# Kernel optimization log

Measured on AMD Instinct MI355X. Metric: run time of the kernel, lower is better.

Reference implementation:

```python
import jax, jax.numpy as jnp
import numpy as np

N_NODES = 100000
MAX_DEG = 128
BATCH = 16384
NUM_SAMPLES = 25


def setup_inputs() -> dict:
    key = jax.random.key(0)
    k1, k2, k3 = jax.random.split(key, 3)
    adj_weight = jax.random.uniform(k1, (N_NODES, MAX_DEG), dtype=jnp.float32)
    adj_info = jax.random.randint(k2, (N_NODES, MAX_DEG), 0, N_NODES, dtype=jnp.int32)
    ids = jax.random.randint(k3, (BATCH,), 0, N_NODES, dtype=jnp.int64)
    return {
        "adj_weight": adj_weight,
        "adj_info": adj_info,
        "ids": ids,
        "num_samples": NUM_SAMPLES,
    }


def reference(adj_weight, adj_info, ids, num_samples):
    # Gather per-node neighbor lists and weights: [B, max_deg]
    adj_lists = adj_info[ids]
    adj_weight_lists = adj_weight[ids]
    # tf.multinomial(tf.log(w), num_samples): categorical sampling with
    # replacement, probabilities proportional to weights.
    logits = jnp.log(adj_weight_lists)  # [B, max_deg]
    skey = jax.random.key(42)
    # categorical over last axis; draw num_samples per row -> [B, num_samples]
    idx = jax.random.categorical(
        skey, logits, axis=-1, shape=(num_samples, ids.shape[0])
    ).T
    # Gather sampled neighbor ids (equivalent to the flattened bias+gather trick)
    res = jnp.take_along_axis(adj_lists, idx, axis=1)  # [B, num_samples]
    return res
```

## Files before the change

kernel.cpp:

```cpp
#include <hip/hip_runtime.h>
#include <stdint.h>


#define MAXDEG 128

__device__ __forceinline__ uint32_t rotl32(uint32_t x, int r) {
  return __builtin_rotateleft32(x, r);
}

__device__ __forceinline__ uint32_t tf_bits(uint32_t i) {
  uint32_t x0, x1;
  x1 = i + 42u;
  x0 = x1;
  x1 = rotl32(x1, 13) ^ x0;
  x0 += x1; x1 = rotl32(x1, 15) ^ x0;
  x0 += x1; x1 = rotl32(x1, 26) ^ x0;
  x0 += x1; x1 = rotl32(x1,  6) ^ x0;
  x1 += 0x1BD11BF1u; x0 = x0 + x1 + 42u;
  x1 = rotl32(x1, 17) ^ x0;
  x0 += x1; x1 = rotl32(x1, 29) ^ x0;
  x0 += x1; x1 = rotl32(x1, 16) ^ x0;
  x0 += x1; x1 = rotl32(x1, 24) ^ x0;
  x1 += 2u; x0 = x0 + x1 + 0x1BD11BF0u;
  x1 = rotl32(x1, 13) ^ x0;
  x0 += x1; x1 = rotl32(x1, 15) ^ x0;
  x0 += x1; x1 = rotl32(x1, 26) ^ x0;
  x0 += x1; x1 = rotl32(x1,  6) ^ x0;
  x1 += 45u; x0 = x0 + x1;
  x1 = rotl32(x1, 17) ^ x0;
  x0 += x1; x1 = rotl32(x1, 29) ^ x0;
  x0 += x1; x1 = rotl32(x1, 16) ^ x0;
  x0 += x1; x1 = rotl32(x1, 24) ^ x0;
  x1 += 0x1BD11BF4u; x0 = x0 + x1 + 42u;
  x1 = rotl32(x1, 13) ^ x0;
  x0 += x1; x1 = rotl32(x1, 15) ^ x0;
  x0 += x1; x1 = rotl32(x1, 26) ^ x0;
  x0 += x1; x1 = rotl32(x1,  6) ^ x0;
  return (x0 + 0x1BD11BF0u) ^ (x1 + 5u);
}

__device__ __forceinline__ float uniform_from_bits(uint32_t bits) {
  uint32_t fb = (bits >> 9) | 0x3f800000u;
  float f = __uint_as_float(fb) - 1.0f;
  return fmaxf(f, 1.17549435e-38f);
}

__device__ __forceinline__ float zscore(float lwp, uint32_t bits) {
  const float l = __log2f(uniform_from_bits(bits));
  const float t = __log2f(-l);
  return __builtin_fmaf(-0.69314718056f, t, lwp);
}

#define SWZMAX(zm, pat) \
  zm = fmaxf(zm, __int_as_float(__builtin_amdgcn_ds_swizzle(__float_as_int(zm), (pat))))

__global__ __launch_bounds__(256) void wns_kernel(
    const float* __restrict__ adj_weight,
    const int* __restrict__ adj_info,
    const int* __restrict__ ids,
    int* __restrict__ out,
    int batch, int nsamp) {
  const int lane = threadIdx.x & 63;
  const int l = lane & 31;
  const int wid = blockIdx.x * 4 + (threadIdx.x >> 6);
  if (2 * wid >= batch) return;
  const int b = 2 * wid + (lane >> 5);

  const long long nid = (long long)ids[b];
  const float4 wv = *(const float4*)(adj_weight + nid * MAXDEG + 4 * l);
  const float lwp0 = __logf(wv.x) + 0.36651292f;
  const float lwp1 = __logf(wv.y) + 0.36651292f;
  const float lwp2 = __logf(wv.z) + 0.36651292f;
  const float lwp3 = __logf(wv.w) + 0.36651292f;

  uint32_t sbase = (uint32_t)b * 128u + (uint32_t)(4 * l);
  const uint32_t sstep = (uint32_t)batch * 128u;

  #pragma unroll 2
  for (int s = 0; s < nsamp; ++s, sbase += sstep) {
    const uint32_t bits0 = tf_bits(sbase + 0u);
    const uint32_t bits1 = tf_bits(sbase + 1u);
    const uint32_t bits2 = tf_bits(sbase + 2u);
    const uint32_t bits3 = tf_bits(sbase + 3u);

    const float z0 = zscore(lwp0, bits0);
    const float z1 = zscore(lwp1, bits1);
    const float z2 = zscore(lwp2, bits2);
    const float z3 = zscore(lwp3, bits3);

    float zmax = fmaxf(fmaxf(fmaxf(z0, z1), z2), z3);
    SWZMAX(zmax, 0x041F);
    SWZMAX(zmax, 0x081F);
    SWZMAX(zmax, 0x101F);
    SWZMAX(zmax, 0x201F);
    SWZMAX(zmax, 0x401F);

    const float thr = zmax - 3.0e-4f;
    const unsigned long long m0 = __ballot(z0 > thr);
    const unsigned long long m1 = __ballot(z1 > thr);
    const unsigned long long m2 = __ballot(z2 > thr);
    const unsigned long long m3 = __ballot(z3 > thr);
    const uint32_t a0 = (uint32_t)m0, a1 = (uint32_t)m1,
                   a2 = (uint32_t)m2, a3 = (uint32_t)m3;
    const uint32_t c0 = (uint32_t)(m0 >> 32), c1 = (uint32_t)(m1 >> 32),
                   c2 = (uint32_t)(m2 >> 32), c3 = (uint32_t)(m3 >> 32);
    const int cntA = __popc(a0) + __popc(a1) + __popc(a2) + __popc(a3);
    const int cntB = __popc(c0) + __popc(c1) + __popc(c2) + __popc(c3);

    int d;
    if (cntA == 1 && cntB == 1) {
      const int dA = a0 ? 4 * __builtin_ctz(a0)
                   : a1 ? 4 * __builtin_ctz(a1) + 1
                   : a2 ? 4 * __builtin_ctz(a2) + 2
                        : 4 * __builtin_ctz(a3) + 3;
      const int dB = c0 ? 4 * __builtin_ctz(c0)
                   : c1 ? 4 * __builtin_ctz(c1) + 1
                   : c2 ? 4 * __builtin_ctz(c2) + 2
                        : 4 * __builtin_ctz(c3) + 3;
      d = (lane < 32) ? dA : dB;
    } else {
      double bz = log((double)wv.x) - log(-log((double)uniform_from_bits(bits0)));
      int bd = 4 * l;
      const double Z1 = log((double)wv.y) - log(-log((double)uniform_from_bits(bits1)));
      if (Z1 > bz) { bz = Z1; bd = 4 * l + 1; }
      const double Z2 = log((double)wv.z) - log(-log((double)uniform_from_bits(bits2)));
      if (Z2 > bz) { bz = Z2; bd = 4 * l + 2; }
      const double Z3 = log((double)wv.w) - log(-log((double)uniform_from_bits(bits3)));
      if (Z3 > bz) { bz = Z3; bd = 4 * l + 3; }
      #pragma unroll
      for (int m = 1; m < 32; m <<= 1) {
        const double oz = __shfl_xor(bz, m);
        const int od = __shfl_xor(bd, m);
        if (oz > bz || (oz == bz && od < bd)) { bz = oz; bd = od; }
      }
      d = bd;
    }

    if (l == 0) {
      out[(long long)b * nsamp + s] = adj_info[nid * MAXDEG + d];
    }
  }
}

extern "C" void kernel_launch(void* const* d_in, const int* in_sizes, int n_in,
                              void* d_out, int out_size, void* d_ws, size_t ws_size,
                              hipStream_t stream) {
  const float* adj_weight = (const float*)d_in[0];
  const int* adj_info = (const int*)d_in[1];
  const int* ids = (const int*)d_in[2];
  int batch = in_sizes[2];
  int nsamp = out_size / batch;
  int waves = (batch + 1) / 2;
  int blocks = (waves + 3) / 4;
  wns_kernel<<<blocks, 256, 0, stream>>>(adj_weight, adj_info, ids,
                                         (int*)d_out, batch, nsamp);
}
```

Before: 153.4 us.

## Defer fp64 tie-break to noinline post-loop pass and use DPP reductions

```diff
diff --git a/kernel.cpp b/kernel.cpp
--- a/kernel.cpp
+++ b/kernel.cpp
@@ -51,10 +51,43 @@
   return __builtin_fmaf(-0.69314718056f, t, lwp);
 }
 
-#define SWZMAX(zm, pat) \
-  zm = fmaxf(zm, __int_as_float(__builtin_amdgcn_ds_swizzle(__float_as_int(zm), (pat))))
+template <int CTRL>
+__device__ __forceinline__ float dpp_max_step(float z) {
+  const int t = __builtin_amdgcn_update_dpp(0, __float_as_int(z), CTRL, 0xF, 0xF, true);
+  return fmaxf(z, __int_as_float(t));
+}
 
-__global__ __launch_bounds__(256) void wns_kernel(
+__device__ __forceinline__ float swz_max16(float z) {
+  return fmaxf(z, __int_as_float(
+      __builtin_amdgcn_ds_swizzle(__float_as_int(z), 0x401F)));
+}
+
+__device__ __attribute__((noinline)) void resolve_f64(
+    float4 wv, uint32_t sbase, int l, int lane, int storeLane,
+    const int* __restrict__ adj_info, long long nid,
+    int* __restrict__ out, long long outIdx) {
+  const uint32_t bits0 = tf_bits(sbase + 0u);
+  const uint32_t bits1 = tf_bits(sbase + 1u);
+  const uint32_t bits2 = tf_bits(sbase + 2u);
+  const uint32_t bits3 = tf_bits(sbase + 3u);
+  double bz = log((double)wv.x) - log(-log((double)uniform_from_bits(bits0)));
+  int bd = 4 * l;
+  const double Z1 = log((double)wv.y) - log(-log((double)uniform_from_bits(bits1)));
+  if (Z1 > bz) { bz = Z1; bd = 4 * l + 1; }
+  const double Z2 = log((double)wv.z) - log(-log((double)uniform_from_bits(bits2)));
+  if (Z2 > bz) { bz = Z2; bd = 4 * l + 2; }
+  const double Z3 = log((double)wv.w) - log(-log((double)uniform_from_bits(bits3)));
+  if (Z3 > bz) { bz = Z3; bd = 4 * l + 3; }
+  #pragma unroll
+  for (int m = 1; m < 32; m <<= 1) {
+    const double oz = __shfl_xor(bz, m);
+    const int od = __shfl_xor(bd, m);
+    if (oz > bz || (oz == bz && od < bd)) { bz = oz; bd = od; }
+  }
+  if (lane == storeLane) out[outIdx] = adj_info[nid * MAXDEG + bd];
+}
+
+__global__ __launch_bounds__(256, 8) void wns_kernel(
     const float* __restrict__ adj_weight,
     const int* __restrict__ adj_info,
     const int* __restrict__ ids,
@@ -76,7 +109,9 @@
   uint32_t sbase = (uint32_t)b * 128u + (uint32_t)(4 * l);
   const uint32_t sstep = (uint32_t)batch * 128u;
 
-  #pragma unroll 2
+  uint32_t flagA = 0u, flagB = 0u;
+
+  #pragma unroll 5
   for (int s = 0; s < nsamp; ++s, sbase += sstep) {
     const uint32_t bits0 = tf_bits(sbase + 0u);
     const uint32_t bits1 = tf_bits(sbase + 1u);
@@ -89,11 +124,11 @@
     const float z3 = zscore(lwp3, bits3);
 
     float zmax = fmaxf(fmaxf(fmaxf(z0, z1), z2), z3);
-    SWZMAX(zmax, 0x041F);
-    SWZMAX(zmax, 0x081F);
-    SWZMAX(zmax, 0x101F);
-    SWZMAX(zmax, 0x201F);
-    SWZMAX(zmax, 0x401F);
+    zmax = dpp_max_step<0x121>(zmax);
+    zmax = dpp_max_step<0x122>(zmax);
+    zmax = dpp_max_step<0x124>(zmax);
+    zmax = dpp_max_step<0x128>(zmax);
+    zmax = swz_max16(zmax);
 
     const float thr = zmax - 3.0e-4f;
     const unsigned long long m0 = __ballot(z0 > thr);
@@ -107,38 +142,31 @@
     const int cntA = __popc(a0) + __popc(a1) + __popc(a2) + __popc(a3);
     const int cntB = __popc(c0) + __popc(c1) + __popc(c2) + __popc(c3);
 
-    int d;
-    if (cntA == 1 && cntB == 1) {
-      const int dA = a0 ? 4 * __builtin_ctz(a0)
-                   : a1 ? 4 * __builtin_ctz(a1) + 1
-                   : a2 ? 4 * __builtin_ctz(a2) + 2
-                        : 4 * __builtin_ctz(a3) + 3;
-      const int dB = c0 ? 4 * __builtin_ctz(c0)
-                   : c1 ? 4 * __builtin_ctz(c1) + 1
-                   : c2 ? 4 * __builtin_ctz(c2) + 2
-                        : 4 * __builtin_ctz(c3) + 3;
-      d = (lane < 32) ? dA : dB;
-    } else {
-      double bz = log((double)wv.x) - log(-log((double)uniform_from_bits(bits0)));
-      int bd = 4 * l;
-      const double Z1 = log((double)wv.y) - log(-log((double)uniform_from_bits(bits1)));
-      if (Z1 > bz) { bz = Z1; bd = 4 * l + 1; }
-      const double Z2 = log((double)wv.z) - log(-log((double)uniform_from_bits(bits2)));
-      if (Z2 > bz) { bz = Z2; bd = 4 * l + 2; }
-      const double Z3 = log((double)wv.w) - log(-log((double)uniform_from_bits(bits3)));
-      if (Z3 > bz) { bz = Z3; bd = 4 * l + 3; }
-      #pragma unroll
-      for (int m = 1; m < 32; m <<= 1) {
-        const double oz = __shfl_xor(bz, m);
-        const int od = __shfl_xor(bd, m);
-        if (oz > bz || (oz == bz && od < bd)) { bz = oz; bd = od; }
-      }
-      d = bd;
-    }
+    const int dA = a0 ? 4 * __builtin_ctz(a0)
+                 : a1 ? 4 * __builtin_ctz(a1) + 1
+                 : a2 ? 4 * __builtin_ctz(a2) + 2
+                 : a3 ? 4 * __builtin_ctz(a3) + 3 : 0;
+    const int dB = c0 ? 4 * __builtin_ctz(c0)
+                 : c1 ? 4 * __builtin_ctz(c1) + 1
+                 : c2 ? 4 * __builtin_ctz(c2) + 2
+                 : c3 ? 4 * __builtin_ctz(c3) + 3 : 0;
+    const int d = (lane < 32) ? dA : dB;
+    if (l == 0) out[(long long)b * nsamp + s] = adj_info[nid * MAXDEG + d];
 
-    if (l == 0) {
-      out[(long long)b * nsamp + s] = adj_info[nid * MAXDEG + d];
-    }
+    flagA |= (cntA != 1) ? (1u << s) : 0u;
+    flagB |= (cntB != 1) ? (1u << s) : 0u;
+  }
+
+  const uint32_t rowbase = (uint32_t)b * 128u + (uint32_t)(4 * l);
+  for (uint32_t m = flagA; m; m &= m - 1u) {
+    const int s = __builtin_ctz(m);
+    resolve_f64(wv, rowbase + (uint32_t)s * sstep, l, lane, 0,
+                adj_info, nid, out, (long long)b * nsamp + s);
+  }
+  for (uint32_t m = flagB; m; m &= m - 1u) {
+    const int s = __builtin_ctz(m);
+    resolve_f64(wv, rowbase + (uint32_t)s * sstep, l, lane, 32,
+                adj_info, nid, out, (long long)b * nsamp + s);
   }
 }
 
```

Result: faster. 148.5 us (-3.2%).
